# Optimization experiments

Hardware: AMD Instinct MI355X
Metric: run time of the kernel (lower is better)

## Reference

```python
import jax, jax.numpy as jnp
import numpy as np

T, B, D, H = 512, 32, 1024, 1024


def setup_inputs() -> dict:
    key = jax.random.key(0)
    k1, k2, k3, k4, k5 = jax.random.split(key, 5)
    s = 1.0 / np.sqrt(H)
    return {
        "input": jax.random.normal(k1, (T, B, D), dtype=jnp.float32),
        "paddings": jnp.zeros((T, B, 1), dtype=jnp.float32),
        "W_ih": jax.random.uniform(k2, (D, 3 * H), jnp.float32, -s, s),
        "W_hh": jax.random.uniform(k3, (H, 3 * H), jnp.float32, -s, s),
        "b_ih": jax.random.uniform(k4, (3 * H,), jnp.float32, -s, s),
        "b_hh": jax.random.uniform(k5, (3 * H,), jnp.float32, -s, s),
    }


def reference(input, paddings, W_ih, W_hh, b_ih, b_hh):
    # GRU cell per step with padding carry-through (padding==1 -> keep prev state).
    def step(h, xp):
        x, p = xp  # x: [B, D], p: [B, 1]
        gi = x @ W_ih + b_ih          # [B, 3H]
        gh = h @ W_hh + b_hh          # [B, 3H]
        i_r, i_z, i_n = jnp.split(gi, 3, axis=-1)
        h_r, h_z, h_n = jnp.split(gh, 3, axis=-1)
        r = jax.nn.sigmoid(i_r + h_r)
        z = jax.nn.sigmoid(i_z + h_z)
        n = jnp.tanh(i_n + r * h_n)
        h_new = (1.0 - z) * n + z * h
        h_new = p * h + (1.0 - p) * h_new
        return h_new, h_new

    h0 = jnp.zeros((input.shape[1], H), dtype=input.dtype)
    h_last, outputs = jax.lax.scan(step, h0, (input, paddings))
    # matches torch module: (stacked outputs, (last output, final state))
    return outputs, (outputs[-1], h_last)
```

## Files before the change

kernel.cpp:

```cpp
#include <hip/hip_runtime.h>
#include <cmath>


typedef short s8v  __attribute__((ext_vector_type(8)));
typedef float f4v  __attribute__((ext_vector_type(4)));

#define NB 64
#define GUARD 16384

__device__ __forceinline__ short f2bf(float f) {
    return __builtin_bit_cast(short, (__bf16)f);
}
__device__ __forceinline__ float bf2f(short s) {
    return (float)__builtin_bit_cast(__bf16, s);
}

__global__ __launch_bounds__(256) void k_transpose_bf16(
        const float* __restrict__ W, short* __restrict__ Wt) {
    __shared__ short Ls[32][72];
    int bk = blockIdx.x & 31;
    int bn = blockIdx.x >> 5;
    int k0 = bk * 32, n0 = bn * 64;
    int tid = threadIdx.x;
    {
        int r  = tid >> 3;
        int c0 = (tid & 7) * 8;
        const float* src = W + (size_t)(k0 + r) * 3072 + n0 + c0;
        float4 f0 = *reinterpret_cast<const float4*>(src);
        float4 f1 = *reinterpret_cast<const float4*>(src + 4);
        Ls[r][c0+0] = f2bf(f0.x); Ls[r][c0+1] = f2bf(f0.y);
        Ls[r][c0+2] = f2bf(f0.z); Ls[r][c0+3] = f2bf(f0.w);
        Ls[r][c0+4] = f2bf(f1.x); Ls[r][c0+5] = f2bf(f1.y);
        Ls[r][c0+6] = f2bf(f1.z); Ls[r][c0+7] = f2bf(f1.w);
    }
    __syncthreads();
    {
        int j   = tid >> 2;
        int kk0 = (tid & 3) * 8;
        s8v v;
        #pragma unroll
        for (int s = 0; s < 8; ++s) v[s] = Ls[kk0 + s][j];
        *reinterpret_cast<s8v*>(Wt + (size_t)(n0 + j) * 1024 + k0 + kk0) = v;
    }
}

__global__ __launch_bounds__(256) void k_gemm_gi(
        const float* __restrict__ X, const short* __restrict__ Wt,
        short* __restrict__ gi) {
    __shared__ short As[128][40];
    __shared__ short Bs[128][40];
    int bm = blockIdx.x & 127;
    int bn = blockIdx.x >> 7;
    int m0 = bm * 128, n0 = bn * 128;
    int tid = threadIdx.x;
    int wid = tid >> 6, l = tid & 63;
    int wm = wid >> 1, wn = wid & 1;
    int lr = l & 15, q = l >> 4;
    f4v acc[4][4] = {};
    int sr = tid >> 1;
    int sc = (tid & 1) * 16;

    for (int kc = 0; kc < 1024; kc += 32) {
        const float* asrc = X + (size_t)(m0 + sr) * 1024 + kc + sc;
        float4 f0 = *reinterpret_cast<const float4*>(asrc);
        float4 f1 = *reinterpret_cast<const float4*>(asrc + 4);
        float4 f2 = *reinterpret_cast<const float4*>(asrc + 8);
        float4 f3 = *reinterpret_cast<const float4*>(asrc + 12);
        s8v av0, av1;
        av0[0]=f2bf(f0.x); av0[1]=f2bf(f0.y); av0[2]=f2bf(f0.z); av0[3]=f2bf(f0.w);
        av0[4]=f2bf(f1.x); av0[5]=f2bf(f1.y); av0[6]=f2bf(f1.z); av0[7]=f2bf(f1.w);
        av1[0]=f2bf(f2.x); av1[1]=f2bf(f2.y); av1[2]=f2bf(f2.z); av1[3]=f2bf(f2.w);
        av1[4]=f2bf(f3.x); av1[5]=f2bf(f3.y); av1[6]=f2bf(f3.z); av1[7]=f2bf(f3.w);
        *reinterpret_cast<s8v*>(&As[sr][sc])     = av0;
        *reinterpret_cast<s8v*>(&As[sr][sc + 8]) = av1;
        const short* bsrc = Wt + (size_t)(n0 + sr) * 1024 + kc + sc;
        *reinterpret_cast<s8v*>(&Bs[sr][sc])     = *reinterpret_cast<const s8v*>(bsrc);
        *reinterpret_cast<s8v*>(&Bs[sr][sc + 8]) = *reinterpret_cast<const s8v*>(bsrc + 8);
        __syncthreads();
        s8v af[4], bf[4];
        #pragma unroll
        for (int ms = 0; ms < 4; ++ms)
            af[ms] = *reinterpret_cast<const s8v*>(&As[wm*64 + ms*16 + lr][q*8]);
        #pragma unroll
        for (int ns = 0; ns < 4; ++ns)
            bf[ns] = *reinterpret_cast<const s8v*>(&Bs[wn*64 + ns*16 + lr][q*8]);
        #pragma unroll
        for (int ms = 0; ms < 4; ++ms)
            #pragma unroll
            for (int ns = 0; ns < 4; ++ns)
                acc[ms][ns] = __builtin_amdgcn_mfma_f32_16x16x32_bf16(
                                  af[ms], bf[ns], acc[ms][ns], 0,0,0);
        __syncthreads();
    }
    #pragma unroll
    for (int ms = 0; ms < 4; ++ms)
      #pragma unroll
      for (int ns = 0; ns < 4; ++ns) {
        int m = m0 + wm*64 + ms*16 + q*4;
        int n = n0 + wn*64 + ns*16 + lr;
        #pragma unroll
        for (int i = 0; i < 4; ++i)
            gi[(size_t)(m + i) * 3072 + n] = f2bf(acc[ms][ns][i]);
      }
}

__global__ __launch_bounds__(128, 1) void k_gru(
        const float* __restrict__ pad,
        const short* __restrict__ gi,
        const short* __restrict__ Whht,
        const float* __restrict__ b_ih,
        const float* __restrict__ b_hh,
        unsigned long long* __restrict__ hb4,
        unsigned* __restrict__ flags,
        float* __restrict__ out) {
    extern __shared__ short wlds[];
    const int WS = 1032;
    int bid = blockIdx.x;
    int j0  = bid * 16;
    int tid = threadIdx.x;
    int w   = tid >> 6;
    int l   = tid & 63, lr = l & 15, q = l >> 4;

    for (int idx = tid; idx < 48 * 128; idx += 128) {
        int row = idx >> 7;
        int ko  = (idx & 127) * 8;
        int g = row >> 4, c = row & 15;
        *reinterpret_cast<s8v*>(&wlds[(g * 16 + c) * WS + ko]) =
            *reinterpret_cast<const s8v*>(Whht + (size_t)(g * 1024 + j0 + c) * 1024 + ko);
    }
    __syncthreads();

    int jq = j0 + q * 4;
    int b  = w * 16 + lr;
    f4v sbr = *reinterpret_cast<const f4v*>(b_ih + jq)
            + *reinterpret_cast<const f4v*>(b_hh + jq);
    f4v sbz = *reinterpret_cast<const f4v*>(b_ih + 1024 + jq)
            + *reinterpret_cast<const f4v*>(b_hh + 1024 + jq);
    f4v sbn_i = *reinterpret_cast<const f4v*>(b_ih + 2048 + jq);
    f4v sbn_h = *reinterpret_cast<const f4v*>(b_hh + 2048 + jq);
    const short* w_r = &wlds[(0 * 16 + lr) * WS + q * 8];
    const short* w_z = &wlds[(1 * 16 + lr) * WS + q * 8];
    const short* w_n = &wlds[(2 * 16 + lr) * WS + q * 8];
    float hp[4] = {0.f, 0.f, 0.f, 0.f};

    const unsigned* myflag = flags + w * 64 + l;

    int m_  = bid * 4 + q;
    int kk_ = ((m_ >> 3) << 1) | (m_ & 1);
    int sl_ = ((m_ & 7) >> 1) * 16 + lr;
    unsigned long long* hw0 = hb4 + (size_t)w * 4096 + kk_ * 64 + sl_;
    unsigned long long* hw1 = hw0 + 8192;
    const unsigned long long* hc0 = hb4 + (size_t)w * 4096 + l;
    const unsigned long long* hc1 = hc0 + 8192;

    union u64s { unsigned long long u; short s[4]; };
    u64s gr_, gz_, gn_; float pv;
    {
        const short* gp = gi + (size_t)b * 3072 + jq;
        gr_.u = *reinterpret_cast<const unsigned long long*>(gp);
        gz_.u = *reinterpret_cast<const unsigned long long*>(gp + 1024);
        gn_.u = *reinterpret_cast<const unsigned long long*>(gp + 2048);
        pv = pad[b];
    }

    for (int t = 0; t < 512; ++t) {
        unsigned uT = (unsigned)t;

        unsigned long long bal;
        {
            unsigned f = __hip_atomic_load(myflag, __ATOMIC_RELAXED,
                                           __HIP_MEMORY_SCOPE_AGENT);
            bal = __ballot((int)(f >= uT));
        }

        const unsigned long long* hbase = (t & 1) ? hc1 : hc0;
        unsigned long long ha[32], hb_[32];
        f4v ar = {0,0,0,0}, az = {0,0,0,0}, an = {0,0,0,0};
        #pragma unroll
        for (int it = 0; it < 36; ++it) {
            if (it < 32) {
                unsigned long long need = 3ull << (2 * it);
                int g1 = 0;
                while ((bal & need) != need) {
                    if (++g1 > GUARD) break;
                    __builtin_amdgcn_s_sleep(1);
                    unsigned f = __hip_atomic_load(myflag, __ATOMIC_RELAXED,
                                                   __HIP_MEMORY_SCOPE_AGENT);
                    bal = __ballot((int)(f >= uT));
                }
                ha[it]  = __hip_atomic_load(hbase + (2*it)     * 64,
                              __ATOMIC_RELAXED, __HIP_MEMORY_SCOPE_AGENT);
                hb_[it] = __hip_atomic_load(hbase + (2*it + 1) * 64,
                              __ATOMIC_RELAXED, __HIP_MEMORY_SCOPE_AGENT);
            }
            if (it >= 4) {
                int jt = it - 4;
                union { unsigned long long u[2]; s8v v; } hx;
                hx.u[0] = ha[jt]; hx.u[1] = hb_[jt];
                s8v r8 = *reinterpret_cast<const s8v*>(w_r + jt * 32);
                s8v z8 = *reinterpret_cast<const s8v*>(w_z + jt * 32);
                s8v n8 = *reinterpret_cast<const s8v*>(w_n + jt * 32);
                ar = __builtin_amdgcn_mfma_f32_16x16x32_bf16(r8, hx.v, ar, 0,0,0);
                az = __builtin_amdgcn_mfma_f32_16x16x32_bf16(z8, hx.v, az, 0,0,0);
                an = __builtin_amdgcn_mfma_f32_16x16x32_bf16(n8, hx.v, an, 0,0,0);
            }
        }

        #pragma unroll
        for (int i = 0; i < 4; ++i) {
            float xr = bf2f(gr_.s[i]) + ar[i] + sbr[i];
            float xz = bf2f(gz_.s[i]) + az[i] + sbz[i];
            float r  = __builtin_amdgcn_rcpf(1.f + __expf(-xr));
            float z  = __builtin_amdgcn_rcpf(1.f + __expf(-xz));
            float xn = bf2f(gn_.s[i]) + sbn_i[i] + r * (an[i] + sbn_h[i]);
            float e2 = __expf(2.f * xn);
            float n  = 1.f - 2.f * __builtin_amdgcn_rcpf(1.f + e2);
            float hnv = (1.f - z) * n + z * hp[i];
            hnv = pv * hp[i] + (1.f - pv) * hnv;
            hp[i] = hnv;
        }

        int rowg = t * 32 + b;

        if (t < 511) {
            u64s pk;
            pk.s[0] = f2bf(hp[0]); pk.s[1] = f2bf(hp[1]);
            pk.s[2] = f2bf(hp[2]); pk.s[3] = f2bf(hp[3]);
            unsigned long long* hwr = ((t + 1) & 1) ? hw1 : hw0;
            __hip_atomic_store(hwr, pk.u, __ATOMIC_RELAXED, __HIP_MEMORY_SCOPE_AGENT);
            __builtin_amdgcn_s_waitcnt(0);
            if (l == 0)
                __hip_atomic_store(flags + w * 64 + bid, (unsigned)(t + 1),
                                   __ATOMIC_RELAXED, __HIP_MEMORY_SCOPE_AGENT);
        }

        float4 o4 = { hp[0], hp[1], hp[2], hp[3] };
        *reinterpret_cast<float4*>(out + (size_t)rowg * 1024 + jq) = o4;
        if (t == 511) {
            *reinterpret_cast<float4*>(out + 16777216 + b * 1024 + jq) = o4;
            *reinterpret_cast<float4*>(out + 16809984 + b * 1024 + jq) = o4;
        }

        if (t < 511) {
            const short* gp = gi + (size_t)((t + 1) * 32 + b) * 3072 + jq;
            gr_.u = *reinterpret_cast<const unsigned long long*>(gp);
            gz_.u = *reinterpret_cast<const unsigned long long*>(gp + 1024);
            gn_.u = *reinterpret_cast<const unsigned long long*>(gp + 2048);
            pv = pad[(t + 1) * 32 + b];
        }
    }
}

extern "C" void kernel_launch(void* const* d_in, const int* in_sizes, int n_in,
                              void* d_out, int out_size, void* d_ws, size_t ws_size,
                              hipStream_t stream) {
    const float* X   = (const float*)d_in[0];
    const float* pad = (const float*)d_in[1];
    const float* Wih = (const float*)d_in[2];
    const float* Whh = (const float*)d_in[3];
    const float* bih = (const float*)d_in[4];
    const float* bhh = (const float*)d_in[5];
    float* out = (float*)d_out;

    char* ws = (char*)d_ws;
    short*    gi    = (short*)(ws);
    short*    Wih_t = (short*)(ws + 100663296);
    short*    Whh_t = (short*)(ws + 106954752);
    unsigned long long* hb4 =
        (unsigned long long*)(ws + 100663296);
    unsigned* flags = (unsigned*)(ws + 100663296 + 131072);

    hipLaunchKernelGGL(k_transpose_bf16, dim3(1536), dim3(256), 0, stream, Wih, Wih_t);
    hipLaunchKernelGGL(k_transpose_bf16, dim3(1536), dim3(256), 0, stream, Whh, Whh_t);
    hipLaunchKernelGGL(k_gemm_gi, dim3(128 * 24), dim3(256), 0, stream, X, Wih_t, gi);

    hipMemsetAsync(hb4, 0, 131072 + 512, stream);

    hipFuncSetAttribute((const void*)k_gru,
                        hipFuncAttributeMaxDynamicSharedMemorySize, 99072);
    hipLaunchKernelGGL(k_gru, dim3(NB), dim3(128), 99072, stream,
                       pad, gi, Whh_t, bih, bhh, hb4, flags, out);
}
```

Baseline: 2.809 ms.

## Replace per-chunk flag polling with one full barrier wait before each step

The fine-grained per-k-chunk readiness polling interleaved with the MFMA loop is removed. Each wave now waits once, after publishing its own hidden-state slice, until all producer flags reach t+1. It then loads the whole hidden vector into 64 registers up front and runs the MFMA chain. The flag snapshot is taken before the store drain, and the output store and next-step gate prefetch are moved ahead of the spin to hide latency. The trade-off is losing the overlap between waiting on late producers and computing on early ones, in exchange for a simpler loop and lower polling overhead. Register pressure also rises.

```diff
diff --git a/kernel.cpp b/kernel.cpp
--- a/kernel.cpp
+++ b/kernel.cpp
@@ -144,6 +144,7 @@
     float hp[4] = {0.f, 0.f, 0.f, 0.f};
 
     const unsigned* myflag = flags + w * 64 + l;
+    int self = (int)(l == (unsigned)bid);
 
     int m_  = bid * 4 + q;
     int kk_ = ((m_ >> 3) << 1) | (m_ & 1);
@@ -164,46 +165,24 @@
     }
 
     for (int t = 0; t < 512; ++t) {
-        unsigned uT = (unsigned)t;
-
-        unsigned long long bal;
-        {
-            unsigned f = __hip_atomic_load(myflag, __ATOMIC_RELAXED,
-                                           __HIP_MEMORY_SCOPE_AGENT);
-            bal = __ballot((int)(f >= uT));
-        }
-
         const unsigned long long* hbase = (t & 1) ? hc1 : hc0;
-        unsigned long long ha[32], hb_[32];
+        unsigned long long hreg[64];
+        #pragma unroll
+        for (int k = 0; k < 64; ++k)
+            hreg[k] = __hip_atomic_load(hbase + (size_t)k * 64,
+                                        __ATOMIC_RELAXED, __HIP_MEMORY_SCOPE_AGENT);
+
         f4v ar = {0,0,0,0}, az = {0,0,0,0}, an = {0,0,0,0};
         #pragma unroll
-        for (int it = 0; it < 36; ++it) {
-            if (it < 32) {
-                unsigned long long need = 3ull << (2 * it);
-                int g1 = 0;
-                while ((bal & need) != need) {
-                    if (++g1 > GUARD) break;
-                    __builtin_amdgcn_s_sleep(1);
-                    unsigned f = __hip_atomic_load(myflag, __ATOMIC_RELAXED,
-                                                   __HIP_MEMORY_SCOPE_AGENT);
-                    bal = __ballot((int)(f >= uT));
-                }
-                ha[it]  = __hip_atomic_load(hbase + (2*it)     * 64,
-                              __ATOMIC_RELAXED, __HIP_MEMORY_SCOPE_AGENT);
-                hb_[it] = __hip_atomic_load(hbase + (2*it + 1) * 64,
-                              __ATOMIC_RELAXED, __HIP_MEMORY_SCOPE_AGENT);
-            }
-            if (it >= 4) {
-                int jt = it - 4;
-                union { unsigned long long u[2]; s8v v; } hx;
-                hx.u[0] = ha[jt]; hx.u[1] = hb_[jt];
-                s8v r8 = *reinterpret_cast<const s8v*>(w_r + jt * 32);
-                s8v z8 = *reinterpret_cast<const s8v*>(w_z + jt * 32);
-                s8v n8 = *reinterpret_cast<const s8v*>(w_n + jt * 32);
-                ar = __builtin_amdgcn_mfma_f32_16x16x32_bf16(r8, hx.v, ar, 0,0,0);
-                az = __builtin_amdgcn_mfma_f32_16x16x32_bf16(z8, hx.v, az, 0,0,0);
-                an = __builtin_amdgcn_mfma_f32_16x16x32_bf16(n8, hx.v, an, 0,0,0);
-            }
+        for (int it = 0; it < 32; ++it) {
+            union { unsigned long long u[2]; s8v v; } hx;
+            hx.u[0] = hreg[2*it]; hx.u[1] = hreg[2*it+1];
+            s8v r8 = *reinterpret_cast<const s8v*>(w_r + it * 32);
+            s8v z8 = *reinterpret_cast<const s8v*>(w_z + it * 32);
+            s8v n8 = *reinterpret_cast<const s8v*>(w_n + it * 32);
+            ar = __builtin_amdgcn_mfma_f32_16x16x32_bf16(r8, hx.v, ar, 0,0,0);
+            az = __builtin_amdgcn_mfma_f32_16x16x32_bf16(z8, hx.v, az, 0,0,0);
+            an = __builtin_amdgcn_mfma_f32_16x16x32_bf16(n8, hx.v, an, 0,0,0);
         }
 
         #pragma unroll
@@ -221,32 +200,45 @@
         }
 
         int rowg = t * 32 + b;
+        float4 o4 = { hp[0], hp[1], hp[2], hp[3] };
 
         if (t < 511) {
+            unsigned uT1 = (unsigned)(t + 1);
+
             u64s pk;
             pk.s[0] = f2bf(hp[0]); pk.s[1] = f2bf(hp[1]);
             pk.s[2] = f2bf(hp[2]); pk.s[3] = f2bf(hp[3]);
             unsigned long long* hwr = ((t + 1) & 1) ? hw1 : hw0;
             __hip_atomic_store(hwr, pk.u, __ATOMIC_RELAXED, __HIP_MEMORY_SCOPE_AGENT);
+            unsigned fsnap = __hip_atomic_load(myflag, __ATOMIC_RELAXED,
+                                               __HIP_MEMORY_SCOPE_AGENT);
             __builtin_amdgcn_s_waitcnt(0);
             if (l == 0)
-                __hip_atomic_store(flags + w * 64 + bid, (unsigned)(t + 1),
+                __hip_atomic_store(flags + w * 64 + bid, uT1,
                                    __ATOMIC_RELAXED, __HIP_MEMORY_SCOPE_AGENT);
-        }
-
-        float4 o4 = { hp[0], hp[1], hp[2], hp[3] };
-        *reinterpret_cast<float4*>(out + (size_t)rowg * 1024 + jq) = o4;
-        if (t == 511) {
+
+            *reinterpret_cast<float4*>(out + (size_t)rowg * 1024 + jq) = o4;
+            {
+                const short* gp = gi + (size_t)((t + 1) * 32 + b) * 3072 + jq;
+                gr_.u = *reinterpret_cast<const unsigned long long*>(gp);
+                gz_.u = *reinterpret_cast<const unsigned long long*>(gp + 1024);
+                gn_.u = *reinterpret_cast<const unsigned long long*>(gp + 2048);
+                pv = pad[(t + 1) * 32 + b];
+            }
+
+            int ok = (int)(fsnap >= uT1) | self;
+            int g1 = 0;
+            while (!__all(ok)) {
+                if (++g1 > GUARD) break;
+                __builtin_amdgcn_s_sleep(1);
+                unsigned f = __hip_atomic_load(myflag, __ATOMIC_RELAXED,
+                                               __HIP_MEMORY_SCOPE_AGENT);
+                ok = (int)(f >= uT1) | self;
+            }
+        } else {
+            *reinterpret_cast<float4*>(out + (size_t)rowg * 1024 + jq) = o4;
             *reinterpret_cast<float4*>(out + 16777216 + b * 1024 + jq) = o4;
             *reinterpret_cast<float4*>(out + 16809984 + b * 1024 + jq) = o4;
-        }
-
-        if (t < 511) {
-            const short* gp = gi + (size_t)((t + 1) * 32 + b) * 3072 + jq;
-            gr_.u = *reinterpret_cast<const unsigned long long*>(gp);
-            gz_.u = *reinterpret_cast<const unsigned long long*>(gp + 1024);
-            gn_.u = *reinterpret_cast<const unsigned long long*>(gp + 2048);
-            pv = pad[(t + 1) * 32 + b];
         }
     }
 }
```

New measurement: 2.678 ms. 4.7% less time.
